# Kernel tuning notes

Hardware: AMD Instinct MI355X
Metric: run time of the kernel (lower is better)

## Reference

```python
import jax, jax.numpy as jnp
import numpy as np

NUM_HEAD = 16
EMB_DIM = 1024
HEAD_DIM = EMB_DIM // NUM_HEAD

def setup_inputs() -> dict:
    key = jax.random.key(0)
    ks = jax.random.split(key, 9)
    B, S, D = 2, 2048, EMB_DIM
    s = 1.0 / np.sqrt(D)
    return {
        "x": jax.random.normal(ks[0], (B, S, D), dtype=jnp.float32),
        "Wq": jax.random.normal(ks[1], (D, D), dtype=jnp.float32) * s,
        "bq": jnp.zeros((D,), dtype=jnp.float32),
        "Wk": jax.random.normal(ks[2], (D, D), dtype=jnp.float32) * s,
        "bk": jnp.zeros((D,), dtype=jnp.float32),
        "Wv": jax.random.normal(ks[3], (D, D), dtype=jnp.float32) * s,
        "bv": jnp.zeros((D,), dtype=jnp.float32),
        "Wo": jax.random.normal(ks[4], (D, D), dtype=jnp.float32) * s,
        "bo": jnp.zeros((D,), dtype=jnp.float32),
    }

def reference(x, Wq, bq, Wk, bk, Wv, bv, Wo, bo):
    B, S, D = x.shape
    H, Hd = NUM_HEAD, HEAD_DIM
    # projections (torch Linear: x @ W.T + b; here W stored as [in, out])
    Q = (x @ Wq + bq).reshape(B, S, H, Hd)
    K = (x @ Wk + bk).reshape(B, S, H, Hd)
    V = (x @ Wv + bv).reshape(B, S, H, Hd)
    scale = jnp.sqrt(jnp.asarray(Hd, dtype=x.dtype))
    scores = jnp.einsum('bqhd,bkhd->bhqk', Q, K) / scale  # [B,H,S,S]
    attn = jax.nn.softmax(scores, axis=-1)
    out = jnp.einsum('bhql,blhd->bqhd', attn, V).reshape(B, S, D)
    return out @ Wo + bo
```

## Files before the change

### kernel.cpp

```cpp
#include <hip/hip_runtime.h>
#include <math.h>


using bf16   = __bf16;
using bf16x8 = __attribute__((ext_vector_type(8))) __bf16;
using bf16x4 = __attribute__((ext_vector_type(4))) __bf16;
using bf16x2 = __attribute__((ext_vector_type(2))) __bf16;
using f32x4  = __attribute__((ext_vector_type(4))) float;

#define MFMA16(a, b, c) __builtin_amdgcn_mfma_f32_16x16x32_bf16((a), (b), (c), 0, 0, 0)
#define WAIT_VM0() asm volatile("s_waitcnt vmcnt(0)" ::: "memory")
#define WAITBAR(N) asm volatile("s_waitcnt vmcnt(" #N ")\n\ts_barrier" ::: "memory")

__device__ __forceinline__ bf16x8 ld8(const bf16* p) { return *(const bf16x8*)p; }

__device__ __forceinline__ void ldg_lds16(bf16* lds_base, const bf16* g) {
    __builtin_amdgcn_global_load_lds(
        (const __attribute__((address_space(1))) void*)g,
        (__attribute__((address_space(3))) void*)lds_base, 16, 0, 0);
}

__device__ __forceinline__ float fast_exp2(float x) {
#if __has_builtin(__builtin_amdgcn_exp2f)
    return __builtin_amdgcn_exp2f(x);
#else
    return exp2f(x);
#endif
}

__device__ __forceinline__ float rowsum16(float v) {
    v += __shfl_xor(v, 1, 64);
    v += __shfl_xor(v, 2, 64);
    v += __shfl_xor(v, 4, 64);
    v += __shfl_xor(v, 8, 64);
    return v;
}

__global__ __launch_bounds__(256) void prep_kernel(
    const float* __restrict__ x, const float* __restrict__ Wq,
    const float* __restrict__ Wk, const float* __restrict__ Wv,
    const float* __restrict__ Wo, bf16* __restrict__ xb,
    bf16* __restrict__ WtBase) {
    const int z = blockIdx.z;
    const int tid = threadIdx.x;
    if (z == 4) {
        int id = blockIdx.y * 32 + blockIdx.x;
#pragma unroll
        for (int k = 0; k < 4; ++k) {
            int i = id * 4096 + k * 1024 + tid * 4;
            float4 v = *(const float4*)&x[i];
            bf16x4 o = { (bf16)v.x, (bf16)v.y, (bf16)v.z, (bf16)v.w };
            *(bf16x4*)&xb[i] = o;
        }
        return;
    }
    __shared__ float tile[32][33];
    const float* W = (z == 0) ? Wq : (z == 1) ? Wk : (z == 2) ? Wv : Wo;
    bf16* Wt = WtBase + (size_t)z * 1024 * 1024;
    const int tx = tid & 31, ty = tid >> 5;
    const int x0 = blockIdx.x * 32, y0 = blockIdx.y * 32;
#pragma unroll
    for (int i = 0; i < 4; ++i)
        tile[ty + i * 8][tx] = W[(size_t)(y0 + ty + i * 8) * 1024 + x0 + tx];
    __syncthreads();
#pragma unroll
    for (int i = 0; i < 4; ++i)
        Wt[(size_t)(x0 + ty + i * 8) * 1024 + y0 + tx] = (bf16)tile[tx][ty + i * 8];
}

__device__ __forceinline__ void gemm_stage(const bf16* __restrict__ src, int r0,
                                           int k0, bf16* dst, int w, int lane) {
#pragma unroll
    for (int c = 0; c < 2; ++c) {
        int flat = (w * 2 + c) * 64 + lane;
        int row = flat >> 2, cc = flat & 3;
        int gk = (cc ^ ((row >> 1) & 3)) * 8;
        ldg_lds16(dst + (size_t)(w * 2 + c) * 512,
                  src + (size_t)(r0 + row) * 1024 + k0 + gk);
    }
}

__device__ __forceinline__ void gemm_core_128(const bf16* __restrict__ A,
                                              const bf16* __restrict__ Bt,
                                              int m0, int n0,
                                              bf16* As, bf16* Bs,
                                              f32x4 (&acc)[4][4]) {
    const int tid = threadIdx.x, lane = tid & 63, w = tid >> 6;
    const int lo = lane & 15, quad = lane >> 4;
    const int wm = w >> 1, wn = w & 1;

    gemm_stage(A,  m0, 0, As, w, lane);
    gemm_stage(Bt, n0, 0, Bs, w, lane);
    WAIT_VM0();
    __syncthreads();

    for (int it = 0; it < 32; ++it) {
        const int buf = it & 1;
        if (it + 1 < 32) {
            gemm_stage(A,  m0, (it + 1) * 32, As + (buf ^ 1) * 4096, w, lane);
            gemm_stage(Bt, n0, (it + 1) * 32, Bs + (buf ^ 1) * 4096, w, lane);
        }
        const bf16* Ab = As + buf * 4096;
        const bf16* Bb = Bs + buf * 4096;
        bf16x8 af[4], bq[4];
#pragma unroll
        for (int t = 0; t < 4; ++t) {
            int r = wm * 64 + t * 16 + lo;
            af[t] = ld8(&Ab[r * 32 + ((quad ^ ((r >> 1) & 3)) * 8)]);
        }
#pragma unroll
        for (int t = 0; t < 4; ++t) {
            int r = wn * 64 + t * 16 + lo;
            bq[t] = ld8(&Bb[r * 32 + ((quad ^ ((r >> 1) & 3)) * 8)]);
        }
#pragma unroll
        for (int mt = 0; mt < 4; ++mt)
#pragma unroll
            for (int nt = 0; nt < 4; ++nt)
                acc[mt][nt] = MFMA16(af[mt], bq[nt], acc[mt][nt]);
        WAIT_VM0();
        __syncthreads();
    }
}

__global__ __launch_bounds__(256, 3) void qkv_gemm_kernel(
    const bf16* __restrict__ Xb, const bf16* __restrict__ Wts,
    const float* __restrict__ bq, const float* __restrict__ bk,
    const float* __restrict__ bv,
    bf16* __restrict__ Qo, bf16* __restrict__ Ko, bf16* __restrict__ Vto) {
    __shared__ bf16 Smem[4 * 4096];
    bf16* As = Smem;
    bf16* Bs = Smem + 2 * 4096;
    const int z = blockIdx.z;
    const bf16*  Bt   = Wts + (size_t)z * 1024 * 1024;
    const float* bias = (z == 0) ? bq : (z == 1) ? bk : bv;
    const int m0 = blockIdx.y * 128, n0 = blockIdx.x * 128;

    f32x4 acc[4][4] = {};
    gemm_core_128(Xb, Bt, m0, n0, As, Bs, acc);

    const int tid = threadIdx.x;
    const int lane = tid & 63, w = tid >> 6;
    const int lo = lane & 15, quad = lane >> 4;
    const int wm = w >> 1, wn = w & 1;
    const float QSCALE = 0.125f * 1.44269504088896f;

    if (z == 2) {
        bf16* T = Smem;
        const int b = m0 >> 11;
        const int s_base = m0 & 2047;
#pragma unroll
        for (int half = 0; half < 2; ++half) {
            __syncthreads();
            if (wm == half) {
#pragma unroll
                for (int nt = 0; nt < 4; ++nt)
#pragma unroll
                    for (int mt = 0; mt < 4; ++mt)
#pragma unroll
                        for (int r = 0; r < 4; ++r) {
                            int nn = wn * 64 + nt * 16 + lo;
                            int mm = mt * 16 + quad * 4 + r;
                            T[nn * 68 + mm] = (bf16)(acc[mt][nt][r] + bias[n0 + nn]);
                        }
            }
            __syncthreads();
#pragma unroll
            for (int p = 0; p < 8; ++p) {
                int pos = p * 1024 + tid * 4;
                int row = pos >> 6, col = pos & 63;
                int n = n0 + row, h = n >> 6, hd = n & 63;
                bf16x4 v = *(const bf16x4*)&T[row * 68 + col];
                *(bf16x4*)&Vto[((size_t)((b * 16 + h) * 64 + hd) << 11)
                               + s_base + half * 64 + col] = v;
            }
        }
    } else {
#pragma unroll
        for (int mt = 0; mt < 4; ++mt)
#pragma unroll
            for (int nt = 0; nt < 4; ++nt)
#pragma unroll
                for (int r = 0; r < 4; ++r) {
                    int m = m0 + wm * 64 + mt * 16 + quad * 4 + r;
                    int n = n0 + wn * 64 + nt * 16 + lo;
                    float v = acc[mt][nt][r] + bias[n];
                    int b = m >> 11, s = m & 2047, h = n >> 6, hd = n & 63;
                    if (z == 0)
                        Qo[((size_t)((b * 16 + h) * 2048 + s) << 6) + hd] = (bf16)(v * QSCALE);
                    else
                        Ko[((size_t)((b * 16 + h) * 2048 + s) << 6) + hd] = (bf16)v;
                }
    }
}

__global__ __launch_bounds__(256, 2) void out_gemm_kernel(
    const bf16* __restrict__ A, const bf16* __restrict__ Bt,
    const float* __restrict__ bo, float* __restrict__ Co) {
    __shared__ bf16 As[2 * 2048];
    __shared__ bf16 Bs[2 * 4096];
    const int tid = threadIdx.x, lane = tid & 63, w = tid >> 6;
    const int lo = lane & 15, quad = lane >> 4;
    const int wm = w >> 1, wn = w & 1;
    const int m0 = blockIdx.y * 64, n0 = blockIdx.x * 128;

    auto stageA = [&](int k0, bf16* dst) {
        int flat = w * 64 + lane;
        int row = flat >> 2, cc = flat & 3;
        int gk = (cc ^ ((row >> 1) & 3)) * 8;
        ldg_lds16(dst + (size_t)w * 512, A + (size_t)(m0 + row) * 1024 + k0 + gk);
    };
    auto stageB = [&](int k0, bf16* dst) {
#pragma unroll
        for (int c = 0; c < 2; ++c) {
            int flat = (w * 2 + c) * 64 + lane;
            int row = flat >> 2, cc = flat & 3;
            int gk = (cc ^ ((row >> 1) & 3)) * 8;
            ldg_lds16(dst + (size_t)(w * 2 + c) * 512,
                      Bt + (size_t)(n0 + row) * 1024 + k0 + gk);
        }
    };

    f32x4 acc[2][4] = {};
    stageA(0, As);
    stageB(0, Bs);
    WAIT_VM0();
    __syncthreads();

    for (int it = 0; it < 32; ++it) {
        const int buf = it & 1;
        if (it + 1 < 32) {
            stageA((it + 1) * 32, As + (buf ^ 1) * 2048);
            stageB((it + 1) * 32, Bs + (buf ^ 1) * 4096);
        }
        const bf16* Ab = As + buf * 2048;
        const bf16* Bb = Bs + buf * 4096;
        bf16x8 af[2], bq[4];
#pragma unroll
        for (int t = 0; t < 2; ++t) {
            int r = wm * 32 + t * 16 + lo;
            af[t] = ld8(&Ab[r * 32 + ((quad ^ ((r >> 1) & 3)) * 8)]);
        }
#pragma unroll
        for (int t = 0; t < 4; ++t) {
            int r = wn * 64 + t * 16 + lo;
            bq[t] = ld8(&Bb[r * 32 + ((quad ^ ((r >> 1) & 3)) * 8)]);
        }
#pragma unroll
        for (int mt = 0; mt < 2; ++mt)
#pragma unroll
            for (int nt = 0; nt < 4; ++nt)
                acc[mt][nt] = MFMA16(af[mt], bq[nt], acc[mt][nt]);
        WAIT_VM0();
        __syncthreads();
    }

#pragma unroll
    for (int mt = 0; mt < 2; ++mt)
#pragma unroll
        for (int nt = 0; nt < 4; ++nt)
#pragma unroll
            for (int r = 0; r < 4; ++r) {
                int m = m0 + wm * 32 + mt * 16 + quad * 4 + r;
                int n = n0 + wn * 64 + nt * 16 + lo;
                Co[(size_t)m * 1024 + n] = acc[mt][nt][r] + bo[n];
            }
}

#define PSTR 36

__global__ __launch_bounds__(256, 2) void attn_kernel(
    const bf16* __restrict__ Q, const bf16* __restrict__ K,
    const bf16* __restrict__ Vt, bf16* __restrict__ AO) {
    __shared__ bf16 Ks[4][32 * 64];
    __shared__ bf16 Vs[4][64 * 32];
    __shared__ bf16 Pl[4][32 * PSTR];
    const int tid = threadIdx.x, w = tid >> 6, lane = tid & 63;
    const int lo = lane & 15, quad = lane >> 4;
    const int blk = blockIdx.x;
    const int bh = (blk & 7) | ((blk >> 7) << 3);
    const int qb = (blk >> 3) & 15;
    const int q0 = qb * 128 + w * 32;

    const bf16* Qb = Q + ((size_t)bh * 2048 + q0) * 64;
    const bf16* Kb = K + (size_t)bh * 2048 * 64;
    const bf16* Vb = Vt + (size_t)bh * 64 * 2048;
    bf16* Pw = &Pl[w][0];

    bf16x8 qa[2][2];
#pragma unroll
    for (int mt = 0; mt < 2; ++mt)
#pragma unroll
        for (int ks = 0; ks < 2; ++ks)
            qa[mt][ks] = ld8(&Qb[(mt * 16 + lo) * 64 + ks * 32 + quad * 8]);

    f32x4 O[2][4] = {};
    f32x4 l_acc[2] = {};

    const int kRow = (w * 64 + lane) >> 3, kCc = lane & 7;
    const int vRow = (w * 64 + lane) >> 2, vCc = lane & 3;
    const int gKo = (kCc ^ ((kRow >> 2) & 7)) * 8;
    const int gVo = (vCc ^ (vRow & 3)) * 8;
    auto stage = [&](int s0, int buf) {
        ldg_lds16(&Ks[buf][w * 512], &Kb[(size_t)(s0 + kRow) * 64 + gKo]);
        ldg_lds16(&Vs[buf][w * 512], &Vb[(size_t)vRow * 2048 + s0 + gVo]);
    };

    stage(0, 0);
    stage(32, 1);
    stage(64, 2);
    WAITBAR(4);

    for (int it = 0; it < 64; ++it) {
        const int buf = it & 3;
        if (it + 3 < 64) stage((it + 3) * 32, (it + 3) & 3);
        const bf16* Kt = &Ks[buf][0];
        const bf16* Vl = &Vs[buf][0];

        f32x4 S[2][2] = {};
#pragma unroll
        for (int t = 0; t < 2; ++t) {
            int r = lo * 2 + t;
            int sw = (r >> 2) & 7;
#pragma unroll
            for (int ks = 0; ks < 2; ++ks) {
                bf16x8 kf = ld8(&Kt[r * 64 + (((quad + 4 * ks) ^ sw) * 8)]);
                S[0][t] = MFMA16(qa[0][ks], kf, S[0][t]);
                S[1][t] = MFMA16(qa[1][ks], kf, S[1][t]);
            }
        }
#pragma unroll
        for (int mt = 0; mt < 2; ++mt)
#pragma unroll
            for (int r = 0; r < 4; ++r) {
                float p0 = fast_exp2(S[mt][0][r]);
                float p1 = fast_exp2(S[mt][1][r]);
                l_acc[mt][r] += p0 + p1;
                bf16x2 pk = { (bf16)p0, (bf16)p1 };
                *(bf16x2*)&Pw[(mt * 16 + quad * 4 + r) * PSTR + lo * 2] = pk;
            }
        bf16x8 vf[4];
#pragma unroll
        for (int nt = 0; nt < 4; ++nt) {
            int r = nt * 16 + lo;
            vf[nt] = ld8(&Vl[r * 32 + ((quad ^ (r & 3)) * 8)]);
        }
#pragma unroll
        for (int mt = 0; mt < 2; ++mt) {
            bf16x8 pa = ld8(&Pw[(mt * 16 + lo) * PSTR + quad * 8]);
#pragma unroll
            for (int nt = 0; nt < 4; ++nt)
                O[mt][nt] = MFMA16(pa, vf[nt], O[mt][nt]);
        }
        if (it < 61)       WAITBAR(4);
        else if (it == 61) WAITBAR(2);
        else if (it == 62) WAITBAR(0);
    }

    const int bb = bh >> 4, h = bh & 15;
#pragma unroll
    for (int mt = 0; mt < 2; ++mt) {
        const size_t outbase = ((size_t)(bb * 2048 + q0 + mt * 16)) * 1024 + h * 64;
#pragma unroll
        for (int r = 0; r < 4; ++r) {
            float rl = 1.0f / rowsum16(l_acc[mt][r]);
            size_t rowoff = outbase + (size_t)(quad * 4 + r) * 1024;
#pragma unroll
            for (int nt = 0; nt < 4; ++nt)
                AO[rowoff + nt * 16 + lo] = (bf16)(O[mt][nt][r] * rl);
        }
    }
}

extern "C" void kernel_launch(void* const* d_in, const int* in_sizes, int n_in,
                              void* d_out, int out_size, void* d_ws, size_t ws_size,
                              hipStream_t stream) {
    const float* x  = (const float*)d_in[0];
    const float* Wq = (const float*)d_in[1];
    const float* bq = (const float*)d_in[2];
    const float* Wk = (const float*)d_in[3];
    const float* bk = (const float*)d_in[4];
    const float* Wv = (const float*)d_in[5];
    const float* bv = (const float*)d_in[6];
    const float* Wo = (const float*)d_in[7];
    const float* bo = (const float*)d_in[8];
    float* out = (float*)d_out;

    bf16* wsb = (bf16*)d_ws;
    const size_t M1 = 1024u * 1024u;
    bf16* Xb  = wsb;
    bf16* AO  = wsb;
    bf16* Wt  = wsb + 4 * M1;
    bf16* Qw  = wsb + 8 * M1;
    bf16* Kw  = wsb + 12 * M1;
    bf16* Vtw = wsb + 16 * M1;

    prep_kernel<<<dim3(32, 32, 5), 256, 0, stream>>>(x, Wq, Wk, Wv, Wo, Xb, Wt);
    qkv_gemm_kernel<<<dim3(8, 32, 3), 256, 0, stream>>>(Xb, Wt, bq, bk, bv, Qw, Kw, Vtw);
    attn_kernel<<<512, 256, 0, stream>>>(Qw, Kw, Vtw, AO);
    out_gemm_kernel<<<dim3(8, 64), 256, 0, stream>>>(AO, Wt + 3 * M1, bo, out);
}
```

Before: 213.2 us.

## Keep softmax probabilities in registers by transposing score MFMA and permuting V layout

The attention kernel now computes S^T (K as the A operand) so each lane's exp'd scores already sit in the register layout needed as the A operand of the PV MFMA. This removes the per-iteration LDS round trip for P. The V projection writes V^T with a permuted column order to match. The K/V tile grows to 64 keys with triple buffering, and occupancy is raised to 3 blocks per CU. The row-sum is reduced across lanes once at the end. In exchange, LDS use per block grows and register pressure rises under the tighter launch bound.

Measured after the change: 181.6 us. 1.17x faster.

```diff
diff --git a/kernel.cpp b/kernel.cpp
--- a/kernel.cpp
+++ b/kernel.cpp
@@ -5,7 +5,6 @@
 using bf16   = __bf16;
 using bf16x8 = __attribute__((ext_vector_type(8))) __bf16;
 using bf16x4 = __attribute__((ext_vector_type(4))) __bf16;
-using bf16x2 = __attribute__((ext_vector_type(2))) __bf16;
 using f32x4  = __attribute__((ext_vector_type(4))) float;
 
 #define MFMA16(a, b, c) __builtin_amdgcn_mfma_f32_16x16x32_bf16((a), (b), (c), 0, 0, 0)
@@ -26,14 +25,6 @@
 #else
     return exp2f(x);
 #endif
-}
-
-__device__ __forceinline__ float rowsum16(float v) {
-    v += __shfl_xor(v, 1, 64);
-    v += __shfl_xor(v, 2, 64);
-    v += __shfl_xor(v, 4, 64);
-    v += __shfl_xor(v, 8, 64);
-    return v;
 }
 
 __global__ __launch_bounds__(256) void prep_kernel(
@@ -170,9 +161,11 @@
                 int pos = p * 1024 + tid * 4;
                 int row = pos >> 6, col = pos & 63;
                 int n = n0 + row, h = n >> 6, hd = n & 63;
+                int colp = (col & 32) | (((col >> 2) & 3) << 3)
+                         | (((col >> 4) & 1) << 2) | (col & 3);
                 bf16x4 v = *(const bf16x4*)&T[row * 68 + col];
                 *(bf16x4*)&Vto[((size_t)((b * 16 + h) * 64 + hd) << 11)
-                               + s_base + half * 64 + col] = v;
+                               + s_base + half * 64 + colp] = v;
             }
         }
     } else {
@@ -267,14 +260,11 @@
             }
 }
 
-#define PSTR 36
-
-__global__ __launch_bounds__(256, 2) void attn_kernel(
+__global__ __launch_bounds__(256, 3) void attn_kernel(
     const bf16* __restrict__ Q, const bf16* __restrict__ K,
     const bf16* __restrict__ Vt, bf16* __restrict__ AO) {
-    __shared__ bf16 Ks[4][32 * 64];
-    __shared__ bf16 Vs[4][64 * 32];
-    __shared__ bf16 Pl[4][32 * PSTR];
+    __shared__ bf16 Ks[3][64 * 64];
+    __shared__ bf16 Vs[3][64 * 64];
     const int tid = threadIdx.x, w = tid >> 6, lane = tid & 63;
     const int lo = lane & 15, quad = lane >> 4;
     const int blk = blockIdx.x;
@@ -285,89 +275,103 @@
     const bf16* Qb = Q + ((size_t)bh * 2048 + q0) * 64;
     const bf16* Kb = K + (size_t)bh * 2048 * 64;
     const bf16* Vb = Vt + (size_t)bh * 64 * 2048;
-    bf16* Pw = &Pl[w][0];
 
     bf16x8 qa[2][2];
 #pragma unroll
-    for (int mt = 0; mt < 2; ++mt)
+    for (int qt = 0; qt < 2; ++qt)
 #pragma unroll
         for (int ks = 0; ks < 2; ++ks)
-            qa[mt][ks] = ld8(&Qb[(mt * 16 + lo) * 64 + ks * 32 + quad * 8]);
+            qa[qt][ks] = ld8(&Qb[(qt * 16 + lo) * 64 + ks * 32 + quad * 8]);
 
     f32x4 O[2][4] = {};
-    f32x4 l_acc[2] = {};
-
-    const int kRow = (w * 64 + lane) >> 3, kCc = lane & 7;
-    const int vRow = (w * 64 + lane) >> 2, vCc = lane & 3;
-    const int gKo = (kCc ^ ((kRow >> 2) & 7)) * 8;
-    const int gVo = (vCc ^ (vRow & 3)) * 8;
+    float l_acc[2] = { 0.f, 0.f };
+
     auto stage = [&](int s0, int buf) {
-        ldg_lds16(&Ks[buf][w * 512], &Kb[(size_t)(s0 + kRow) * 64 + gKo]);
-        ldg_lds16(&Vs[buf][w * 512], &Vb[(size_t)vRow * 2048 + s0 + gVo]);
+#pragma unroll
+        for (int c = 0; c < 2; ++c) {
+            int flat = (w * 2 + c) * 64 + lane;
+            int row = flat >> 3, cc = flat & 7;
+            int g = (cc ^ (row & 7)) * 8;
+            ldg_lds16(&Ks[buf][(w * 2 + c) * 512], &Kb[(size_t)(s0 + row) * 64 + g]);
+            ldg_lds16(&Vs[buf][(w * 2 + c) * 512], &Vb[(size_t)row * 2048 + s0 + g]);
+        }
     };
 
+    const int swz = lo & 7;
+
+    auto body = [&](int rbuf) {
+        const bf16* Kt = &Ks[rbuf][0];
+        const bf16* Vl = &Vs[rbuf][0];
+        f32x4 S[2][4] = {};
+#pragma unroll
+        for (int t = 0; t < 4; ++t) {
+            int r = t * 16 + lo;
+#pragma unroll
+            for (int ks = 0; ks < 2; ++ks) {
+                bf16x8 kf = ld8(&Kt[r * 64 + (((quad + 4 * ks) ^ swz) * 8)]);
+                S[0][t] = MFMA16(kf, qa[0][ks], S[0][t]);
+                S[1][t] = MFMA16(kf, qa[1][ks], S[1][t]);
+            }
+        }
+        bf16x8 pa[2][2];
+#pragma unroll
+        for (int qt = 0; qt < 2; ++qt)
+#pragma unroll
+            for (int kc = 0; kc < 2; ++kc) {
+                float e0 = fast_exp2(S[qt][2 * kc][0]);
+                float e1 = fast_exp2(S[qt][2 * kc][1]);
+                float e2 = fast_exp2(S[qt][2 * kc][2]);
+                float e3 = fast_exp2(S[qt][2 * kc][3]);
+                float e4 = fast_exp2(S[qt][2 * kc + 1][0]);
+                float e5 = fast_exp2(S[qt][2 * kc + 1][1]);
+                float e6 = fast_exp2(S[qt][2 * kc + 1][2]);
+                float e7 = fast_exp2(S[qt][2 * kc + 1][3]);
+                l_acc[qt] += ((e0 + e1) + (e2 + e3)) + ((e4 + e5) + (e6 + e7));
+                pa[qt][kc] = bf16x8{ (bf16)e0, (bf16)e1, (bf16)e2, (bf16)e3,
+                                     (bf16)e4, (bf16)e5, (bf16)e6, (bf16)e7 };
+            }
+#pragma unroll
+        for (int kc = 0; kc < 2; ++kc)
+#pragma unroll
+            for (int nt = 0; nt < 4; ++nt) {
+                int r = nt * 16 + lo;
+                bf16x8 vf = ld8(&Vl[r * 64 + ((((kc * 4 + quad) ^ swz)) * 8)]);
+                O[0][nt] = MFMA16(pa[0][kc], vf, O[0][nt]);
+                O[1][nt] = MFMA16(pa[1][kc], vf, O[1][nt]);
+            }
+    };
+
     stage(0, 0);
-    stage(32, 1);
-    stage(64, 2);
+    stage(64, 1);
     WAITBAR(4);
 
-    for (int it = 0; it < 64; ++it) {
-        const int buf = it & 3;
-        if (it + 3 < 64) stage((it + 3) * 32, (it + 3) & 3);
-        const bf16* Kt = &Ks[buf][0];
-        const bf16* Vl = &Vs[buf][0];
-
-        f32x4 S[2][2] = {};
-#pragma unroll
-        for (int t = 0; t < 2; ++t) {
-            int r = lo * 2 + t;
-            int sw = (r >> 2) & 7;
-#pragma unroll
-            for (int ks = 0; ks < 2; ++ks) {
-                bf16x8 kf = ld8(&Kt[r * 64 + (((quad + 4 * ks) ^ sw) * 8)]);
-                S[0][t] = MFMA16(qa[0][ks], kf, S[0][t]);
-                S[1][t] = MFMA16(qa[1][ks], kf, S[1][t]);
-            }
-        }
-#pragma unroll
-        for (int mt = 0; mt < 2; ++mt)
-#pragma unroll
-            for (int r = 0; r < 4; ++r) {
-                float p0 = fast_exp2(S[mt][0][r]);
-                float p1 = fast_exp2(S[mt][1][r]);
-                l_acc[mt][r] += p0 + p1;
-                bf16x2 pk = { (bf16)p0, (bf16)p1 };
-                *(bf16x2*)&Pw[(mt * 16 + quad * 4 + r) * PSTR + lo * 2] = pk;
-            }
-        bf16x8 vf[4];
-#pragma unroll
-        for (int nt = 0; nt < 4; ++nt) {
-            int r = nt * 16 + lo;
-            vf[nt] = ld8(&Vl[r * 32 + ((quad ^ (r & 3)) * 8)]);
-        }
-#pragma unroll
-        for (int mt = 0; mt < 2; ++mt) {
-            bf16x8 pa = ld8(&Pw[(mt * 16 + lo) * PSTR + quad * 8]);
+    int rbuf = 0, sbuf = 2;
+    for (int it = 0; it < 30; ++it) {
+        stage((it + 2) * 64, sbuf);
+        sbuf = (sbuf == 2) ? 0 : sbuf + 1;
+        body(rbuf);
+        WAITBAR(4);
+        rbuf = (rbuf == 2) ? 0 : rbuf + 1;
+    }
+    body(rbuf);
+    WAITBAR(0);
+    rbuf = (rbuf == 2) ? 0 : rbuf + 1;
+    body(rbuf);
+
+    const int bb = bh >> 4, h = bh & 15;
+#pragma unroll
+    for (int qt = 0; qt < 2; ++qt) {
+        float lt = l_acc[qt];
+        lt += __shfl_xor(lt, 16, 64);
+        lt += __shfl_xor(lt, 32, 64);
+        const size_t outbase = ((size_t)(bb * 2048 + q0 + qt * 16)) * 1024 + h * 64;
+#pragma unroll
+        for (int r = 0; r < 4; ++r) {
+            float rl = 1.0f / __shfl(lt, quad * 4 + r, 64);
+            size_t rowoff = outbase + (size_t)(quad * 4 + r) * 1024;
 #pragma unroll
             for (int nt = 0; nt < 4; ++nt)
-                O[mt][nt] = MFMA16(pa, vf[nt], O[mt][nt]);
-        }
-        if (it < 61)       WAITBAR(4);
-        else if (it == 61) WAITBAR(2);
-        else if (it == 62) WAITBAR(0);
-    }
-
-    const int bb = bh >> 4, h = bh & 15;
-#pragma unroll
-    for (int mt = 0; mt < 2; ++mt) {
-        const size_t outbase = ((size_t)(bb * 2048 + q0 + mt * 16)) * 1024 + h * 64;
-#pragma unroll
-        for (int r = 0; r < 4; ++r) {
-            float rl = 1.0f / rowsum16(l_acc[mt][r]);
-            size_t rowoff = outbase + (size_t)(quad * 4 + r) * 1024;
-#pragma unroll
-            for (int nt = 0; nt < 4; ++nt)
-                AO[rowoff + nt * 16 + lo] = (bf16)(O[mt][nt][r] * rl);
+                AO[rowoff + nt * 16 + lo] = (bf16)(O[qt][nt][r] * rl);
         }
     }
 }
```
